# Kernel optimization log

Hardware: AMD Instinct MI355X
Metric: run time of the kernel (lower is better)

## Reference

```python
import jax, jax.numpy as jnp
import numpy as np

D_MODEL = 2048
N_HEADS = 16
HEAD_DIM = D_MODEL // N_HEADS  # 128


def setup_inputs() -> dict:
    key = jax.random.key(0)
    ks = jax.random.split(key, 7)
    B, S, CACHE = 2, 2048, 2048
    scale = 1.0 / np.sqrt(D_MODEL)
    return {
        "x": jax.random.normal(ks[0], (B, S, D_MODEL), dtype=jnp.float32),
        "cached_k": jax.random.normal(ks[1], (B, N_HEADS, CACHE, HEAD_DIM), dtype=jnp.float32),
        "cached_v": jax.random.normal(ks[2], (B, N_HEADS, CACHE, HEAD_DIM), dtype=jnp.float32),
        "W_q": jax.random.normal(ks[3], (D_MODEL, D_MODEL), dtype=jnp.float32) * scale,
        "W_k": jax.random.normal(ks[4], (D_MODEL, D_MODEL), dtype=jnp.float32) * scale,
        "W_v": jax.random.normal(ks[5], (D_MODEL, D_MODEL), dtype=jnp.float32) * scale,
        "W_o": jax.random.normal(ks[6], (D_MODEL, D_MODEL), dtype=jnp.float32) * scale,
    }


def reference(x, cached_k, cached_v, W_q, W_k, W_v, W_o):
    B, S, _ = x.shape
    # nn.Linear(d,d,bias=False): y = x @ W.T
    def proj(W):
        h = jnp.einsum("bsd,ed->bse", x, W)
        return h.reshape(B, S, N_HEADS, HEAD_DIM).transpose(0, 2, 1, 3)  # (B,H,S,Dh)
    q = proj(W_q)
    k = jnp.concatenate([cached_k, proj(W_k)], axis=2)  # (B,H,T,Dh)
    v = jnp.concatenate([cached_v, proj(W_v)], axis=2)
    scores = jnp.einsum("bhsd,bhtd->bhst", q, k) / np.sqrt(HEAD_DIM)
    attn = jax.nn.softmax(scores, axis=-1)
    out = jnp.einsum("bhst,bhtd->bhsd", attn, v)  # (B,H,S,Dh)
    out = out.transpose(0, 2, 1, 3).reshape(B, S, D_MODEL)
    out = jnp.einsum("bsd,ed->bse", out, W_o)
    return out, k, v
```

## Files before the change

### kernel.cpp

```cpp
#include <hip/hip_runtime.h>

typedef __bf16 bf16;
typedef __bf16 bf16x4 __attribute__((ext_vector_type(4)));
typedef __bf16 bf16x8 __attribute__((ext_vector_type(8)));
typedef float f32x4 __attribute__((ext_vector_type(4)));
typedef float f32x16 __attribute__((ext_vector_type(16)));
typedef int iv2 __attribute__((ext_vector_type(2)));

#define LOG2E 1.44269504088896340736f
#define QSCALE 0.12751884935f
#define RESCALE_THR 8.0f

__device__ __forceinline__ void gload_lds16(const void* gp, void* lp) {
    __builtin_amdgcn_global_load_lds(
        (__attribute__((address_space(1))) void*)gp,
        (__attribute__((address_space(3))) void*)lp,
        16, 0, 0);
}

__device__ __forceinline__ int swz(int j, int row) {
    return (j & 8) | ((j ^ row) & 7);
}

__device__ __forceinline__ unsigned cvtpk(float lo, float hi) {
    unsigned w;
    asm("v_cvt_pk_bf16_f32 %0, %1, %2" : "=v"(w) : "v"(lo), "v"(hi));
    return w;
}

__device__ __forceinline__ iv2 permswap(unsigned a, unsigned b) {
    return __builtin_amdgcn_permlane32_swap((int)a, (int)b, false, false);
}
__device__ __forceinline__ float halfmax(float v) {
    iv2 r = permswap(__float_as_uint(v), __float_as_uint(v));
    return fmaxf(__int_as_float(r[0]), __int_as_float(r[1]));
}
__device__ __forceinline__ float halfadd(float v) {
    iv2 r = permswap(__float_as_uint(v), __float_as_uint(v));
    return __int_as_float(r[0]) + __int_as_float(r[1]);
}

__device__ __forceinline__ float vmax32(const f32x16& a, const f32x16& b) {
    float t[8];
    #pragma unroll
    for (int i = 0; i < 8; ++i)
        t[i] = fmaxf(fmaxf(a[i], a[i + 8]), fmaxf(b[i], b[i + 8]));
    return fmaxf(fmaxf(fmaxf(t[0], t[1]), fmaxf(t[2], t[3])),
                 fmaxf(fmaxf(t[4], t[5]), fmaxf(t[6], t[7])));
}
__device__ __forceinline__ float vsum32(const f32x16& a, const f32x16& b) {
    float t[8];
    #pragma unroll
    for (int i = 0; i < 8; ++i)
        t[i] = (a[i] + a[i + 8]) + (b[i] + b[i + 8]);
    return ((t[0] + t[1]) + (t[2] + t[3])) + ((t[4] + t[5]) + (t[6] + t[7]));
}

__global__ void conv_bf16(const float* __restrict__ in, bf16* __restrict__ out, int n4) {
    int i = blockIdx.x * 256 + threadIdx.x;
    if (i < n4) {
        float4 f = ((const float4*)in)[i];
        bf16x4 v;
        v[0] = (bf16)f.x; v[1] = (bf16)f.y; v[2] = (bf16)f.z; v[3] = (bf16)f.w;
        *(bf16x4*)(out + (size_t)i * 4) = v;
    }
}

__global__ void copy_cache_k(const float* __restrict__ ck, float* __restrict__ kout,
                             bf16* __restrict__ kb) {
    size_t i = ((size_t)blockIdx.x * 256 + threadIdx.x) * 4;
    size_t bh  = i >> 18;
    size_t rem = i & 262143;
    size_t o   = (bh << 19) + rem;
    float4 f = *(const float4*)(ck + i);
    *(float4*)(kout + o) = f;
    bf16x4 v;
    v[0] = (bf16)f.x; v[1] = (bf16)f.y; v[2] = (bf16)f.z; v[3] = (bf16)f.w;
    *(bf16x4*)(kb + o) = v;
}

__global__ void copy_cache_v(const float* __restrict__ cv, float* __restrict__ vout,
                             bf16* __restrict__ vtb) {
    __shared__ float tile[32][33];
    int bh = blockIdx.z;
    int t0 = blockIdx.x * 32;
    int dh0 = blockIdx.y * 32;
    int tx = threadIdx.x, ty = threadIdx.y;
    const float* src = cv + (size_t)bh * 2048 * 128;
    float* dstf = vout + (size_t)bh * 4096 * 128;
    #pragma unroll
    for (int i = 0; i < 4; ++i) {
        int t = t0 + ty * 4 + i;
        float val = src[(size_t)t * 128 + dh0 + tx];
        dstf[(size_t)t * 128 + dh0 + tx] = val;
        tile[ty * 4 + i][tx] = val;
    }
    __syncthreads();
    bf16* dstb = vtb + (size_t)bh * 128 * 4096;
    #pragma unroll
    for (int i = 0; i < 4; ++i) {
        int dh = dh0 + ty * 4 + i;
        dstb[(size_t)dh * 4096 + t0 + tx] = (bf16)tile[tx][ty * 4 + i];
    }
}

template <int MODE>
__global__ __launch_bounds__(256)
void gemm_nt(const bf16* __restrict__ A, const bf16* __restrict__ Bm,
             float* __restrict__ out_f32, bf16* __restrict__ out_bf16) {
    const int K = 2048, N = 2048;
    __shared__ __align__(16) char smem[32768];
    const int tid = threadIdx.x;
    const int wid = tid >> 6;
    const int lane = tid & 63;
    const int quad = lane >> 4;
    const int l16 = lane & 15;
    const int m0 = blockIdx.y * 128;
    const int n0 = blockIdx.x * 128;
    const int wm = (wid & 1) * 64;
    const int wn = (wid >> 1) * 64;

    f32x4 zero = {0.f, 0.f, 0.f, 0.f};
    f32x4 acc[4][4];
    #pragma unroll
    for (int i = 0; i < 4; ++i)
        #pragma unroll
        for (int j = 0; j < 4; ++j) acc[i][j] = zero;

    auto stage = [&](int k0, int buf) {
        char* base = smem + buf * 16384;
        #pragma unroll
        for (int t = 0; t < 2; ++t) {
            int c = t * 256 + tid;
            int row = c >> 2, kc = c & 3;
            const char* gA = (const char*)(A + (size_t)(m0 + row) * K + k0 + kc * 8);
            const char* gB = (const char*)(Bm + (size_t)(n0 + row) * K + k0 + kc * 8);
            char* lA = base + (size_t)(t * 256 + (tid & ~63)) * 16;
            char* lB = base + 8192 + (size_t)(t * 256 + (tid & ~63)) * 16;
            gload_lds16(gA, lA);
            gload_lds16(gB, lB);
        }
    };

    stage(0, 0);
    __syncthreads();

    for (int k0 = 0; k0 < K; k0 += 32) {
        const int cur = (k0 >> 5) & 1;
        if (k0 + 32 < K) stage(k0 + 32, cur ^ 1);
        const char* base = smem + cur * 16384;
        bf16x8 af[4], bfv[4];
        #pragma unroll
        for (int i = 0; i < 4; ++i) {
            af[i]  = *(const bf16x8*)(base + ((wm + i * 16 + l16) * 32 + quad * 8) * 2);
            bfv[i] = *(const bf16x8*)(base + 8192 + ((wn + i * 16 + l16) * 32 + quad * 8) * 2);
        }
        __builtin_amdgcn_s_setprio(1);
        #pragma unroll
        for (int i = 0; i < 4; ++i)
            #pragma unroll
            for (int j = 0; j < 4; ++j)
                acc[i][j] = __builtin_amdgcn_mfma_f32_16x16x32_bf16(af[i], bfv[j], acc[i][j], 0, 0, 0);
        __builtin_amdgcn_s_setprio(0);
        __syncthreads();
    }

    #pragma unroll
    for (int i = 0; i < 4; ++i)
        #pragma unroll
        for (int j = 0; j < 4; ++j)
            #pragma unroll
            for (int r = 0; r < 4; ++r) {
                int grow = m0 + wm + i * 16 + quad * 4 + r;
                int gcol = n0 + wn + j * 16 + l16;
                float v = acc[i][j][r];
                if (MODE == 0) {
                    out_f32[(size_t)grow * N + gcol] = v;
                } else {
                    int b = grow >> 11, s = grow & 2047;
                    int h = gcol >> 7, dh = gcol & 127;
                    if (MODE == 1) {
                        out_bf16[(((size_t)(b * 16 + h) * 2048) + s) * 128 + dh] = (bf16)(v * QSCALE);
                    } else if (MODE == 2) {
                        size_t idx = (((size_t)(b * 16 + h) * 4096) + 2048 + s) * 128 + dh;
                        out_f32[idx] = v;
                        out_bf16[idx] = (bf16)v;
                    } else {
                        size_t idx = (((size_t)(b * 16 + h) * 4096) + 2048 + s) * 128 + dh;
                        out_f32[idx] = v;
                        out_bf16[(((size_t)(b * 16 + h) * 128) + dh) * 4096 + 2048 + s] = (bf16)v;
                    }
                }
            }
}

__global__ __launch_bounds__(256, 2)
void flash_attn(const bf16* __restrict__ qb, const bf16* __restrict__ kb,
                const bf16* __restrict__ vtb, bf16* __restrict__ ab) {
    __shared__ __align__(16) char smem[65536];
    const int tid = threadIdx.x;
    const int wid = tid >> 6;
    const int lane = tid & 63;
    const int hh = lane >> 5;
    const int l31 = lane & 31;

    const int flat = blockIdx.x;
    const int xcd = flat & 7;
    const int idx = flat >> 3;
    const int bh = xcd * 4 + (idx >> 4);
    const int qblk = idx & 15;
    const int b = bh >> 4, h = bh & 15;
    const int s0 = qblk * 128 + wid * 32;

    const bf16* Q  = qb  + (size_t)bh * 2048 * 128;
    const bf16* Kp = kb  + (size_t)bh * 4096 * 128;
    const bf16* Vt = vtb + (size_t)bh * 128 * 4096;

    bf16x8 qf[8];
    #pragma unroll
    for (int ks = 0; ks < 8; ++ks)
        qf[ks] = *(const bf16x8*)(Q + (size_t)(s0 + l31) * 128 + ks * 16 + hh * 8);

    f32x16 oacc[4];
    #pragma unroll
    for (int dhb = 0; dhb < 4; ++dhb)
        #pragma unroll
        for (int i = 0; i < 16; ++i) oacc[dhb][i] = 0.f;
    float mrun = -1e30f, lrun = 0.f;

    auto stage = [&](int t0, int buf) {
        char* Kb = smem + buf * 32768;
        char* Vb = Kb + 16384;
        #pragma unroll
        for (int r = 0; r < 4; ++r) {
            int kc = r * 256 + tid;
            int row = kc >> 4, p = kc & 15;
            int j = swz(p, row);
            gload_lds16(Kp + (size_t)(t0 + row) * 128 + j * 8, Kb + kc * 16);
        }
        #pragma unroll
        for (int r = 0; r < 4; ++r) {
            int vc = r * 256 + tid;
            int row = vc >> 3, p = vc & 7;
            int j = (p ^ row) & 7;
            gload_lds16(Vt + (size_t)row * 4096 + t0 + j * 8, Vb + vc * 16);
        }
    };

    stage(0, 0);
    __syncthreads();

    for (int t0 = 0; t0 < 4096; t0 += 64) {
        const int cur = (t0 >> 6) & 1;
        if (t0 + 64 < 4096) stage(t0 + 64, cur ^ 1);
        const char* Ksh = smem + cur * 32768;
        const char* Vsh = Ksh + 16384;

        f32x16 sacc[2];
        #pragma unroll
        for (int i = 0; i < 16; ++i) { sacc[0][i] = 0.f; sacc[1][i] = 0.f; }
        __builtin_amdgcn_s_setprio(1);
        #pragma unroll
        for (int ks = 0; ks < 8; ++ks) {
            const int r0 = l31, r1 = 32 + l31;
            bf16x8 kf0 = *(const bf16x8*)(Ksh + r0 * 256 + swz(ks * 2 + hh, r0) * 16);
            bf16x8 kf1 = *(const bf16x8*)(Ksh + r1 * 256 + swz(ks * 2 + hh, r1) * 16);
            sacc[0] = __builtin_amdgcn_mfma_f32_32x32x16_bf16(kf0, qf[ks], sacc[0], 0, 0, 0);
            sacc[1] = __builtin_amdgcn_mfma_f32_32x32x16_bf16(kf1, qf[ks], sacc[1], 0, 0, 0);
        }
        __builtin_amdgcn_s_setprio(0);

        float mx = halfmax(vmax32(sacc[0], sacc[1]));
        if (!__all(mx <= mrun + RESCALE_THR)) {
            float mnew = fmaxf(mrun, mx);
            float alpha = __builtin_amdgcn_exp2f(mrun - mnew);
            #pragma unroll
            for (int dhb = 0; dhb < 4; ++dhb)
                #pragma unroll
                for (int i = 0; i < 16; ++i) oacc[dhb][i] *= alpha;
            lrun *= alpha;
            mrun = mnew;
        }
        #pragma unroll
        for (int tb = 0; tb < 2; ++tb)
            #pragma unroll
            for (int i = 0; i < 16; ++i)
                sacc[tb][i] = __builtin_amdgcn_exp2f(sacc[tb][i] - mrun);
        lrun += halfadd(vsum32(sacc[0], sacc[1]));

        bf16x8 pf[4];
        #pragma unroll
        for (int tb = 0; tb < 2; ++tb)
            #pragma unroll
            for (int ksl = 0; ksl < 2; ++ksl) {
                const int g0 = ksl * 8;
                unsigned wa0 = cvtpk(sacc[tb][g0 + 0], sacc[tb][g0 + 1]);
                unsigned wb0 = cvtpk(sacc[tb][g0 + 4], sacc[tb][g0 + 5]);
                unsigned wa1 = cvtpk(sacc[tb][g0 + 2], sacc[tb][g0 + 3]);
                unsigned wb1 = cvtpk(sacc[tb][g0 + 6], sacc[tb][g0 + 7]);
                iv2 r0 = permswap(wa0, wb0);
                iv2 r1 = permswap(wa1, wb1);
                union { int u[4]; bf16x8 v; } pk;
                pk.u[0] = r0[0]; pk.u[1] = r1[0]; pk.u[2] = r0[1]; pk.u[3] = r1[1];
                pf[tb * 2 + ksl] = pk.v;
            }

        __builtin_amdgcn_s_setprio(1);
        #pragma unroll
        for (int dhb = 0; dhb < 4; ++dhb) {
            const int row = dhb * 32 + l31;
            #pragma unroll
            for (int ks = 0; ks < 4; ++ks) {
                bf16x8 vf = *(const bf16x8*)(Vsh + row * 128 + (((ks * 2 + hh) ^ row) & 7) * 16);
                oacc[dhb] = __builtin_amdgcn_mfma_f32_32x32x16_bf16(vf, pf[ks], oacc[dhb], 0, 0, 0);
            }
        }
        __builtin_amdgcn_s_setprio(0);

        __syncthreads();
    }

    const float inv = 1.0f / lrun;
    const int s = s0 + l31;
    #pragma unroll
    for (int dhb = 0; dhb < 4; ++dhb)
        #pragma unroll
        for (int g = 0; g < 4; ++g) {
            bf16x4 o4;
            #pragma unroll
            for (int r = 0; r < 4; ++r) o4[r] = (bf16)(oacc[dhb][g * 4 + r] * inv);
            int dh = dhb * 32 + g * 8 + hh * 4;
            *(bf16x4*)(ab + ((size_t)(b * 2048 + s)) * 2048 + h * 128 + dh) = o4;
        }
}

extern "C" void kernel_launch(void* const* d_in, const int* in_sizes, int n_in,
                              void* d_out, int out_size, void* d_ws, size_t ws_size,
                              hipStream_t stream) {
    const float* x        = (const float*)d_in[0];
    const float* cached_k = (const float*)d_in[1];
    const float* cached_v = (const float*)d_in[2];
    const float* W_q      = (const float*)d_in[3];
    const float* W_k      = (const float*)d_in[4];
    const float* W_v      = (const float*)d_in[5];
    const float* W_o      = (const float*)d_in[6];

    float* out  = (float*)d_out;
    float* kout = out + 8388608;
    float* vout = out + 25165824;

    char* ws = (char*)d_ws;
    size_t off = 0;
    auto alloc = [&](size_t elts) { bf16* p = (bf16*)(ws + off); off += elts * 2; return p; };
    bf16* xb  = alloc(8388608);
    bf16* wqb = alloc(4194304);
    bf16* wkb = alloc(4194304);
    bf16* wvb = alloc(4194304);
    bf16* wob = alloc(4194304);
    bf16* qb  = alloc(8388608);
    bf16* kb  = alloc(16777216);
    bf16* vtb = alloc(16777216);
    bf16* ab  = alloc(8388608);

    conv_bf16<<<8192, 256, 0, stream>>>(x, xb, 2097152);
    conv_bf16<<<4096, 256, 0, stream>>>(W_q, wqb, 1048576);
    conv_bf16<<<4096, 256, 0, stream>>>(W_k, wkb, 1048576);
    conv_bf16<<<4096, 256, 0, stream>>>(W_v, wvb, 1048576);
    conv_bf16<<<4096, 256, 0, stream>>>(W_o, wob, 1048576);
    copy_cache_k<<<8192, 256, 0, stream>>>(cached_k, kout, kb);
    copy_cache_v<<<dim3(64, 4, 32), dim3(32, 8), 0, stream>>>(cached_v, vout, vtb);

    gemm_nt<1><<<dim3(16, 32), 256, 0, stream>>>(xb, wqb, nullptr, qb);
    gemm_nt<2><<<dim3(16, 32), 256, 0, stream>>>(xb, wkb, kout, kb);
    gemm_nt<3><<<dim3(16, 32), 256, 0, stream>>>(xb, wvb, vout, vtb);

    flash_attn<<<512, 256, 0, stream>>>(qb, kb, vtb, ab);

    gemm_nt<0><<<dim3(16, 32), 256, 0, stream>>>(ab, wob, out, nullptr);
}
```

Before: 655.0 us.

## Fuse QKV GEMMs and conversions, add XCD-aware tile remap, reswizzle attention LDS

Merges the five fp32-to-bf16 conversion launches into a single kernel and the three Q/K/V projection GEMMs into one 1536-block launch over a concatenated weight matrix (the weights are contiguous in the workspace). Both GEMMs gain an XCD-aware block-index remap meant to improve L2 reuse. In flash attention, the K and V tiles get a new XOR swizzle, and the V tile is laid out as 64 rows of 256 bytes, to reduce LDS bank conflicts. This cuts launch overhead and tail effects, but the extra per-element branching in the fused epilogue may add some cost.

```diff
diff --git a/kernel.cpp b/kernel.cpp
--- a/kernel.cpp
+++ b/kernel.cpp
@@ -18,8 +18,8 @@
         16, 0, 0);
 }
 
-__device__ __forceinline__ int swz(int j, int row) {
-    return (j & 8) | ((j ^ row) & 7);
+__device__ __forceinline__ int kmask(int r) {
+    return (r & 15) ^ (((r >> 5) & 1) << 2);
 }
 
 __device__ __forceinline__ unsigned cvtpk(float lo, float hi) {
@@ -56,14 +56,27 @@
     return ((t[0] + t[1]) + (t[2] + t[3])) + ((t[4] + t[5]) + (t[6] + t[7]));
 }
 
-__global__ void conv_bf16(const float* __restrict__ in, bf16* __restrict__ out, int n4) {
-    int i = blockIdx.x * 256 + threadIdx.x;
-    if (i < n4) {
-        float4 f = ((const float4*)in)[i];
-        bf16x4 v;
-        v[0] = (bf16)f.x; v[1] = (bf16)f.y; v[2] = (bf16)f.z; v[3] = (bf16)f.w;
-        *(bf16x4*)(out + (size_t)i * 4) = v;
-    }
+__global__ void conv_all(const float* __restrict__ x, const float* __restrict__ wq,
+                         const float* __restrict__ wk, const float* __restrict__ wv,
+                         const float* __restrict__ wo, bf16* __restrict__ xb,
+                         bf16* __restrict__ wbase) {
+    int id = blockIdx.x;
+    const float* src;
+    bf16* dst;
+    int i;
+    if (id < 8192) {
+        src = x; dst = xb;
+        i = id * 256 + threadIdx.x;
+    } else {
+        int w = (id - 8192) >> 12;
+        src = (w == 0) ? wq : (w == 1) ? wk : (w == 2) ? wv : wo;
+        dst = wbase + (size_t)w * 4194304;
+        i = ((id - 8192) & 4095) * 256 + threadIdx.x;
+    }
+    float4 f = ((const float4*)src)[i];
+    bf16x4 v;
+    v[0] = (bf16)f.x; v[1] = (bf16)f.y; v[2] = (bf16)f.z; v[3] = (bf16)f.w;
+    *(bf16x4*)(dst + (size_t)i * 4) = v;
 }
 
 __global__ void copy_cache_k(const float* __restrict__ ck, float* __restrict__ kout,
@@ -104,19 +117,21 @@
     }
 }
 
-template <int MODE>
 __global__ __launch_bounds__(256)
-void gemm_nt(const bf16* __restrict__ A, const bf16* __restrict__ Bm,
-             float* __restrict__ out_f32, bf16* __restrict__ out_bf16) {
-    const int K = 2048, N = 2048;
+void gemm_qkv(const bf16* __restrict__ A, const bf16* __restrict__ Bm,
+              float* __restrict__ kout, float* __restrict__ vout,
+              bf16* __restrict__ qb, bf16* __restrict__ kb, bf16* __restrict__ vtb) {
+    const int K = 2048;
     __shared__ __align__(16) char smem[32768];
     const int tid = threadIdx.x;
     const int wid = tid >> 6;
     const int lane = tid & 63;
     const int quad = lane >> 4;
     const int l16 = lane & 15;
-    const int m0 = blockIdx.y * 128;
-    const int n0 = blockIdx.x * 128;
+    const int wg = blockIdx.x;
+    const int wgid = (wg & 7) * 192 + (wg >> 3);
+    const int m0 = (wgid / 48) * 128;
+    const int n0 = (wgid % 48) * 128;
     const int wm = (wid & 1) * 64;
     const int wn = (wid >> 1) * 64;
 
@@ -165,6 +180,7 @@
         __syncthreads();
     }
 
+    const int seg = n0 >> 11;
     #pragma unroll
     for (int i = 0; i < 4; ++i)
         #pragma unroll
@@ -174,23 +190,94 @@
                 int grow = m0 + wm + i * 16 + quad * 4 + r;
                 int gcol = n0 + wn + j * 16 + l16;
                 float v = acc[i][j][r];
-                if (MODE == 0) {
-                    out_f32[(size_t)grow * N + gcol] = v;
+                int b = grow >> 11, s = grow & 2047;
+                int c2 = gcol & 2047;
+                int h = c2 >> 7, dh = c2 & 127;
+                if (seg == 0) {
+                    qb[(((size_t)(b * 16 + h) * 2048) + s) * 128 + dh] = (bf16)(v * QSCALE);
+                } else if (seg == 1) {
+                    size_t idx = (((size_t)(b * 16 + h) * 4096) + 2048 + s) * 128 + dh;
+                    kout[idx] = v;
+                    kb[idx] = (bf16)v;
                 } else {
-                    int b = grow >> 11, s = grow & 2047;
-                    int h = gcol >> 7, dh = gcol & 127;
-                    if (MODE == 1) {
-                        out_bf16[(((size_t)(b * 16 + h) * 2048) + s) * 128 + dh] = (bf16)(v * QSCALE);
-                    } else if (MODE == 2) {
-                        size_t idx = (((size_t)(b * 16 + h) * 4096) + 2048 + s) * 128 + dh;
-                        out_f32[idx] = v;
-                        out_bf16[idx] = (bf16)v;
-                    } else {
-                        size_t idx = (((size_t)(b * 16 + h) * 4096) + 2048 + s) * 128 + dh;
-                        out_f32[idx] = v;
-                        out_bf16[(((size_t)(b * 16 + h) * 128) + dh) * 4096 + 2048 + s] = (bf16)v;
-                    }
+                    size_t idx = (((size_t)(b * 16 + h) * 4096) + 2048 + s) * 128 + dh;
+                    vout[idx] = v;
+                    vtb[(((size_t)(b * 16 + h) * 128) + dh) * 4096 + 2048 + s] = (bf16)v;
                 }
+            }
+}
+
+__global__ __launch_bounds__(256)
+void gemm_out(const bf16* __restrict__ A, const bf16* __restrict__ Bm,
+              float* __restrict__ out_f32) {
+    const int K = 2048, N = 2048;
+    __shared__ __align__(16) char smem[32768];
+    const int tid = threadIdx.x;
+    const int wid = tid >> 6;
+    const int lane = tid & 63;
+    const int quad = lane >> 4;
+    const int l16 = lane & 15;
+    const int wg = blockIdx.x;
+    const int wgid = (wg & 7) * 64 + (wg >> 3);
+    const int m0 = (wgid >> 4) * 128;
+    const int n0 = (wgid & 15) * 128;
+    const int wm = (wid & 1) * 64;
+    const int wn = (wid >> 1) * 64;
+
+    f32x4 zero = {0.f, 0.f, 0.f, 0.f};
+    f32x4 acc[4][4];
+    #pragma unroll
+    for (int i = 0; i < 4; ++i)
+        #pragma unroll
+        for (int j = 0; j < 4; ++j) acc[i][j] = zero;
+
+    auto stage = [&](int k0, int buf) {
+        char* base = smem + buf * 16384;
+        #pragma unroll
+        for (int t = 0; t < 2; ++t) {
+            int c = t * 256 + tid;
+            int row = c >> 2, kc = c & 3;
+            const char* gA = (const char*)(A + (size_t)(m0 + row) * K + k0 + kc * 8);
+            const char* gB = (const char*)(Bm + (size_t)(n0 + row) * K + k0 + kc * 8);
+            char* lA = base + (size_t)(t * 256 + (tid & ~63)) * 16;
+            char* lB = base + 8192 + (size_t)(t * 256 + (tid & ~63)) * 16;
+            gload_lds16(gA, lA);
+            gload_lds16(gB, lB);
+        }
+    };
+
+    stage(0, 0);
+    __syncthreads();
+
+    for (int k0 = 0; k0 < K; k0 += 32) {
+        const int cur = (k0 >> 5) & 1;
+        if (k0 + 32 < K) stage(k0 + 32, cur ^ 1);
+        const char* base = smem + cur * 16384;
+        bf16x8 af[4], bfv[4];
+        #pragma unroll
+        for (int i = 0; i < 4; ++i) {
+            af[i]  = *(const bf16x8*)(base + ((wm + i * 16 + l16) * 32 + quad * 8) * 2);
+            bfv[i] = *(const bf16x8*)(base + 8192 + ((wn + i * 16 + l16) * 32 + quad * 8) * 2);
+        }
+        __builtin_amdgcn_s_setprio(1);
+        #pragma unroll
+        for (int i = 0; i < 4; ++i)
+            #pragma unroll
+            for (int j = 0; j < 4; ++j)
+                acc[i][j] = __builtin_amdgcn_mfma_f32_16x16x32_bf16(af[i], bfv[j], acc[i][j], 0, 0, 0);
+        __builtin_amdgcn_s_setprio(0);
+        __syncthreads();
+    }
+
+    #pragma unroll
+    for (int i = 0; i < 4; ++i)
+        #pragma unroll
+        for (int j = 0; j < 4; ++j)
+            #pragma unroll
+            for (int r = 0; r < 4; ++r) {
+                int grow = m0 + wm + i * 16 + quad * 4 + r;
+                int gcol = n0 + wn + j * 16 + l16;
+                out_f32[(size_t)grow * N + gcol] = acc[i][j][r];
             }
 }
 
@@ -232,18 +319,20 @@
         char* Kb = smem + buf * 32768;
         char* Vb = Kb + 16384;
         #pragma unroll
-        for (int r = 0; r < 4; ++r) {
-            int kc = r * 256 + tid;
+        for (int r4 = 0; r4 < 4; ++r4) {
+            int kc = r4 * 256 + tid;
             int row = kc >> 4, p = kc & 15;
-            int j = swz(p, row);
+            int j = p ^ kmask(row);
             gload_lds16(Kp + (size_t)(t0 + row) * 128 + j * 8, Kb + kc * 16);
         }
         #pragma unroll
-        for (int r = 0; r < 4; ++r) {
-            int vc = r * 256 + tid;
-            int row = vc >> 3, p = vc & 7;
-            int j = (p ^ row) & 7;
-            gload_lds16(Vt + (size_t)row * 4096 + t0 + j * 8, Vb + vc * 16);
+        for (int r4 = 0; r4 < 4; ++r4) {
+            int vc = r4 * 256 + tid;
+            int row = vc >> 4, j = vc & 15;
+            int g = j ^ kmask(row);
+            int dh = row + (g >> 3) * 64;
+            int p = g & 7;
+            gload_lds16(Vt + (size_t)dh * 4096 + t0 + p * 8, Vb + vc * 16);
         }
     };
 
@@ -262,9 +351,10 @@
         __builtin_amdgcn_s_setprio(1);
         #pragma unroll
         for (int ks = 0; ks < 8; ++ks) {
+            const int c = ks * 2 + hh;
             const int r0 = l31, r1 = 32 + l31;
-            bf16x8 kf0 = *(const bf16x8*)(Ksh + r0 * 256 + swz(ks * 2 + hh, r0) * 16);
-            bf16x8 kf1 = *(const bf16x8*)(Ksh + r1 * 256 + swz(ks * 2 + hh, r1) * 16);
+            bf16x8 kf0 = *(const bf16x8*)(Ksh + r0 * 256 + (c ^ kmask(r0)) * 16);
+            bf16x8 kf1 = *(const bf16x8*)(Ksh + r1 * 256 + (c ^ kmask(r1)) * 16);
             sacc[0] = __builtin_amdgcn_mfma_f32_32x32x16_bf16(kf0, qf[ks], sacc[0], 0, 0, 0);
             sacc[1] = __builtin_amdgcn_mfma_f32_32x32x16_bf16(kf1, qf[ks], sacc[1], 0, 0, 0);
         }
@@ -308,10 +398,11 @@
         __builtin_amdgcn_s_setprio(1);
         #pragma unroll
         for (int dhb = 0; dhb < 4; ++dhb) {
-            const int row = dhb * 32 + l31;
+            const int rr = ((dhb & 1) << 5) + l31;
             #pragma unroll
             for (int ks = 0; ks < 4; ++ks) {
-                bf16x8 vf = *(const bf16x8*)(Vsh + row * 128 + (((ks * 2 + hh) ^ row) & 7) * 16);
+                const int g = (dhb >> 1) * 8 + ks * 2 + hh;
+                bf16x8 vf = *(const bf16x8*)(Vsh + rr * 256 + (g ^ kmask(rr)) * 16);
                 oacc[dhb] = __builtin_amdgcn_mfma_f32_32x32x16_bf16(vf, pf[ks], oacc[dhb], 0, 0, 0);
             }
         }
@@ -361,20 +452,15 @@
     bf16* kb  = alloc(16777216);
     bf16* vtb = alloc(16777216);
     bf16* ab  = alloc(8388608);
-
-    conv_bf16<<<8192, 256, 0, stream>>>(x, xb, 2097152);
-    conv_bf16<<<4096, 256, 0, stream>>>(W_q, wqb, 1048576);
-    conv_bf16<<<4096, 256, 0, stream>>>(W_k, wkb, 1048576);
-    conv_bf16<<<4096, 256, 0, stream>>>(W_v, wvb, 1048576);
-    conv_bf16<<<4096, 256, 0, stream>>>(W_o, wob, 1048576);
+    (void)wkb; (void)wvb;
+
+    conv_all<<<24576, 256, 0, stream>>>(x, W_q, W_k, W_v, W_o, xb, wqb);
     copy_cache_k<<<8192, 256, 0, stream>>>(cached_k, kout, kb);
     copy_cache_v<<<dim3(64, 4, 32), dim3(32, 8), 0, stream>>>(cached_v, vout, vtb);
 
-    gemm_nt<1><<<dim3(16, 32), 256, 0, stream>>>(xb, wqb, nullptr, qb);
-    gemm_nt<2><<<dim3(16, 32), 256, 0, stream>>>(xb, wkb, kout, kb);
-    gemm_nt<3><<<dim3(16, 32), 256, 0, stream>>>(xb, wvb, vout, vtb);
+    gemm_qkv<<<1536, 256, 0, stream>>>(xb, wqb, kout, vout, qb, kb, vtb);
 
     flash_attn<<<512, 256, 0, stream>>>(qb, kb, vtb, ab);
 
-    gemm_nt<0><<<dim3(16, 32), 256, 0, stream>>>(ab, wob, out, nullptr);
-}
+    gemm_out<<<512, 256, 0, stream>>>(ab, wob, out);
+}
```

New measurement: 650.6 us. About the same (-0.7%).
